# Kernel optimization log

Measured on AMD Instinct MI355X. Metric: run time of the kernel, lower is better.

The kernel has to match this reference:

```python
import jax, jax.numpy as jnp
import numpy as np

NUM_GROUPS = 4   # temporal frames == deformable groups
K = 3            # deformable / fusion kernel size
PAD = 1
MAX_DISP = 7
STRIDE2 = 2


def _conv2d(x, w):
    # 3x3, stride 1, pad 1, no bias, NCHW/OIHW
    return jax.lax.conv_general_dilated(
        x, w, window_strides=(1, 1), padding=((PAD, PAD), (PAD, PAD)),
        dimension_numbers=("NCHW", "OIHW", "NCHW"))


def _correlation(x1, x2):
    """FlowNet/PWC correlation: kernel_size=1, max_displacement=7, stride1=1, stride2=2.
    Output: [B, 49, H, W], mean over channels of shifted dot products."""
    B, C, H, W = x1.shape
    r = MAX_DISP // STRIDE2          # 3 -> 7x7 displacement grid
    m = r * STRIDE2                  # 6 = max shift magnitude
    x2p = jnp.pad(x2, ((0, 0), (0, 0), (m, m), (m, m)))
    outs = []
    for di in range(-r, r + 1):
        for dj in range(-r, r + 1):
            dy, dx = di * STRIDE2, dj * STRIDE2
            sh = x2p[:, :, m + dy:m + dy + H, m + dx:m + dx + W]
            outs.append(jnp.mean(x1 * sh, axis=1))
    return jnp.stack(outs, axis=1)   # [B, 49, H, W]


def _deform_conv(x, offset, weight):
    """Deformable conv v1 (ConvOffset2d): 3x3, stride 1, pad 1, NUM_GROUPS deformable groups.
    offset: [B, G*2*K*K, H, W] laid out as (g, k, {dy,dx})."""
    B, C, H, W = x.shape
    G, K2 = NUM_GROUPS, K * K
    Cg = C // G
    off = offset.reshape(B, G, K2, 2, H, W)
    rel = (jnp.arange(K) - PAD).astype(x.dtype)
    rel_y = jnp.repeat(rel, K).reshape(1, 1, K2, 1, 1)   # kh-major, matches weight flatten
    rel_x = jnp.tile(rel, K).reshape(1, 1, K2, 1, 1)
    iy = jnp.arange(H, dtype=x.dtype).reshape(1, 1, 1, H, 1)
    ix = jnp.arange(W, dtype=x.dtype).reshape(1, 1, 1, 1, W)
    py = iy + rel_y + off[:, :, :, 0]   # [B,G,K2,H,W] sample rows
    px = ix + rel_x + off[:, :, :, 1]   # sample cols
    xg = x.reshape(B, G, Cg, H, W).transpose(0, 1, 3, 4, 2)  # [B,G,H,W,Cg]
    y0 = jnp.floor(py); x0 = jnp.floor(px)
    fy = py - y0; fx = px - x0
    y0 = y0.astype(jnp.int32); x0 = x0.astype(jnp.int32)
    bi = jnp.arange(B).reshape(B, 1, 1, 1, 1)
    gi = jnp.arange(G).reshape(1, G, 1, 1, 1)
    acc = jnp.zeros((B, G, K2, H, W, Cg), x.dtype)
    for dy in (0, 1):
        for dx in (0, 1):
            yy = y0 + dy; xx = x0 + dx
            wgt = (fy if dy else 1.0 - fy) * (fx if dx else 1.0 - fx)
            valid = ((yy >= 0) & (yy < H) & (xx >= 0) & (xx < W)).astype(x.dtype)
            v = xg[bi, gi, jnp.clip(yy, 0, H - 1), jnp.clip(xx, 0, W - 1)]
            acc = acc + v * (wgt * valid)[..., None]
    wr = weight.reshape(weight.shape[0], G, Cg, K2)  # [O,G,Cg,K2]
    return jnp.einsum('bgkhwc,ogck->bohw', acc, wr)


def setup_inputs() -> dict:
    key = jax.random.key(0)
    k0, k1, k2, k3 = jax.random.split(key, 4)
    B, C, H, W = 4, 256, 64, 64
    G = NUM_GROUPS
    inputs = jax.random.normal(k0, (B * G, C, H, W), jnp.float32)
    w_offset = jax.random.normal(k1, (G * 2 * K * K, C + MAX_DISP ** 2, K, K), jnp.float32) * 0.02
    w_def = jax.random.normal(k2, (C, C, K, K), jnp.float32) * 0.02
    w_fusion = jax.random.normal(k3, (C, C * G, K, K), jnp.float32) * 0.02
    return {"inputs": inputs, "w_offset": w_offset, "w_def": w_def,
            "w_fusion": w_fusion, "d1": 0, "d2": 0}


def reference(inputs, w_offset, w_def, w_fusion, d1, d2):
    # d1, d2 are unused by the original forward.
    G = NUM_GROUPS
    y = inputs[G - 1::G]
    _y = jax.lax.stop_gradient(y)
    feats = []
    for ii in range(G - 1):           # n_iter = 1
        x = inputs[ii::G]
        _x = jax.lax.stop_gradient(x)
        corr = _correlation(_x, _y)                       # [B,49,H,W]
        off = _conv2d(jnp.concatenate([x, corr], axis=1), w_offset)
        x = _deform_conv(x, off, w_def)
        feats.append(x)
    return _conv2d(jnp.concatenate(feats + [y], axis=1), w_fusion)
```

## Files before the change

kernel.cpp:

```cpp
#include <hip/hip_runtime.h>

#define HH 64
#define WW 64
#define HW 4096
#define CC 256
#define BB 4
#define GG 4
#define NPAIR 3

typedef __attribute__((ext_vector_type(8))) short short8;
typedef __attribute__((ext_vector_type(4))) float f32x4;
typedef unsigned short ushort_t;

__device__ inline ushort_t f2bf(float x) {
    unsigned int u = __float_as_uint(x);
    unsigned int r = (u + 0x7fffu + ((u >> 16) & 1u)) >> 16;
    return (ushort_t)r;
}
__device__ inline float bflo(unsigned u) { return __uint_as_float(u << 16); }
__device__ inline float bfhi(unsigned u) { return __uint_as_float(u & 0xffff0000u); }

__global__ void prep_wdef(const float* __restrict__ wd, ushort_t* __restrict__ wmf) {
    int idx = blockIdx.x * 256 + threadIdx.x;
    if (idx >= 9 * 256 * 256) return;
    int k = idx >> 16;
    int rem = idx & 65535;
    int o = rem >> 8;
    int c = rem & 255;
    wmf[idx] = f2bf(wd[((size_t)(o * 256 + c)) * 9 + k]);
}

__global__ void prep_woff(const float* __restrict__ wo, ushort_t* __restrict__ wmf) {
    int idx = blockIdx.x * 256 + threadIdx.x;
    if (idx >= 9 * 80 * 320) return;
    int k = idx / (80 * 320);
    int rem = idx % (80 * 320);
    int o = rem / 320;
    int ci = rem % 320;
    wmf[idx] = (o < 72 && ci < 305) ? f2bf(wo[((size_t)o * 305 + ci) * 9 + k]) : (ushort_t)0;
}

__global__ void prep_wfus(const float* __restrict__ wf, ushort_t* __restrict__ wmf) {
    int idx = blockIdx.x * 256 + threadIdx.x;
    if (idx >= 9 * 256 * 1024) return;
    int k = idx / (256 * 1024);
    int rem = idx % (256 * 1024);
    int o = rem / 1024;
    int ci = rem % 1024;
    wmf[idx] = f2bf(wf[((size_t)o * 1024 + ci) * 9 + k]);
}

__global__ void __launch_bounds__(256) xt_build(const float* __restrict__ in,
                                                ushort_t* __restrict__ XT) {
    __shared__ ushort_t tileT[64][72];
    int hw0 = blockIdx.x * 64;
    int ct = blockIdx.y;
    int z = blockIdx.z;
    int pair = z >> 2, b = z & 3;
    int t = threadIdx.x;
    int cil = t >> 2, q = t & 3;
    const float* sp = in + ((size_t)(b * 4 + pair) * 256 + ct * 64 + cil) * HW + hw0 + q * 16;
#pragma unroll
    for (int i = 0; i < 16; ++i) tileT[q * 16 + i][cil] = f2bf(sp[i]);
    __syncthreads();
    int hwl = t >> 2;
    const uint4* tp = reinterpret_cast<const uint4*>(&tileT[hwl][q * 16]);
    uint4* op = reinterpret_cast<uint4*>(
        &XT[((size_t)z * HW + hw0 + hwl) * 320 + ct * 64 + q * 16]);
    op[0] = tp[0];
    op[1] = tp[1];
}

__global__ void __launch_bounds__(256, 8) corr_partial(const float* __restrict__ in,
                                                       float* __restrict__ P) {
    __shared__ float x1l[8][64];
    __shared__ float x2l[8][7][76];
    int h = blockIdx.x, z = blockIdx.y, cg = blockIdx.z;
    int pair = z >> 2, b = z & 3;
    const float* x1 = in + (size_t)(b * GG + pair) * CC * HW + h * WW;
    const float* x2 = in + (size_t)(b * GG + 3) * CC * HW;
    int tid = threadIdx.x;
    int w = tid & 63;
    int dg = tid >> 6;

    float acc[2][7];
#pragma unroll
    for (int i = 0; i < 2; ++i)
#pragma unroll
        for (int j = 0; j < 7; ++j) acc[i][j] = 0.f;

    for (int c0 = cg * 64; c0 < cg * 64 + 64; c0 += 8) {
        __syncthreads();
#pragma unroll
        for (int idx = tid; idx < 512; idx += 256) {
            int cc = idx >> 6, ww = idx & 63;
            x1l[cc][ww] = x1[(size_t)(c0 + cc) * HW + ww];
        }
        for (int idx = tid; idx < 8 * 7 * 76; idx += 256) {
            int cc = idx / 532;
            int rem = idx - cc * 532;
            int r = rem / 76;
            int cl = rem - r * 76;
            int row = h + 2 * (r - 3);
            int col = cl - 6;
            float v = 0.f;
            if (row >= 0 && row < HH && col >= 0 && col < WW)
                v = x2[(size_t)(c0 + cc) * HW + row * WW + col];
            x2l[cc][r][cl] = v;
        }
        __syncthreads();
#pragma unroll
        for (int cc = 0; cc < 8; ++cc) {
            float x1v = x1l[cc][w];
#pragma unroll
            for (int i = 0; i < 2; ++i) {
                int di = dg * 2 + i;
                if (di < 7) {
#pragma unroll
                    for (int dj = 0; dj < 7; ++dj)
                        acc[i][dj] += x1v * x2l[cc][di][w + 2 * dj];
                }
            }
        }
    }
    float* pp = P + ((size_t)(cg * 12 + z) * 49) * HW + h * WW + w;
#pragma unroll
    for (int i = 0; i < 2; ++i) {
        int di = dg * 2 + i;
        if (di < 7) {
#pragma unroll
            for (int dj = 0; dj < 7; ++dj)
                pp[(size_t)(di * 7 + dj) * HW] = acc[i][dj];
        }
    }
}

__global__ void __launch_bounds__(256) corr_reduce(const float* __restrict__ P,
                                                   ushort_t* __restrict__ XT) {
    int h = blockIdx.x, z = blockIdx.y;
    int tid = threadIdx.x;
    int w = tid & 63;
    int dg = tid >> 6;
    const size_t cgs = (size_t)12 * 49 * HW;
    ushort_t* xrow = XT + ((size_t)z * HW + h * WW + w) * 320;
#pragma unroll
    for (int i = 0; i < 2; ++i) {
        int di = dg * 2 + i;
        if (di < 7) {
#pragma unroll
            for (int dj = 0; dj < 7; ++dj) {
                int d = di * 7 + dj;
                const float* pp = P + ((size_t)z * 49 + d) * HW + h * WW + w;
                float s = pp[0] + pp[cgs] + pp[2 * cgs] + pp[3 * cgs];
                xrow[256 + d] = f2bf(s * (1.f / 256.f));
            }
        }
    }
    if (dg == 3) {
#pragma unroll
        for (int p = 0; p < 15; ++p) xrow[305 + p] = 0;
    }
}

__global__ void __launch_bounds__(256, 2) offconv_mfma(const ushort_t* __restrict__ XT,
                                                       const ushort_t* __restrict__ wmf,
                                                       float* __restrict__ off) {
    __shared__ ushort_t a_lds[80][40];
    __shared__ ushort_t b_lds[128][40];
    int n0 = blockIdx.x * 128;
    int z = blockIdx.y;
    int t = threadIdx.x;
    int wid = t >> 6;
    int lane = t & 63;
    int l15 = lane & 15;
    int kq = lane >> 4;
    int r2 = t >> 1, half = t & 1;
    int hwB = n0 + r2;
    int hB = hwB >> 6, wB = hwB & 63;
    const ushort_t* xtb = XT + (size_t)z * HW * 320;

    f32x4 acc[5][2];
#pragma unroll
    for (int m = 0; m < 5; ++m)
#pragma unroll
        for (int n = 0; n < 2; ++n) acc[m][n] = (f32x4){0.f, 0.f, 0.f, 0.f};

    for (int tap = 0; tap < 9; ++tap) {
        int kh = tap / 3;
        int kw = tap - kh * 3;
        int hP = hB + kh - 1;
        int wP = wB + kw - 1;
        bool valid = (hP >= 0) && (hP < HH) && (wP >= 0) && (wP < WW);
        const ushort_t* brow = xtb + (size_t)(hP * WW + wP) * 320;
#pragma unroll 1
        for (int cs = 0; cs < 10; ++cs) {
            int ci0 = cs * 32;
            uint4 vb0 = make_uint4(0, 0, 0, 0), vb1 = make_uint4(0, 0, 0, 0);
            if (valid) {
                const uint4* gp = reinterpret_cast<const uint4*>(brow + ci0 + half * 16);
                vb0 = gp[0];
                vb1 = gp[1];
            }
            uint4 va0, va1;
            if (t < 160) {
                const uint4* ga = reinterpret_cast<const uint4*>(
                    wmf + ((size_t)tap * 80 + r2) * 320 + ci0 + half * 16);
                va0 = ga[0];
                va1 = ga[1];
            }
            __syncthreads();
            {
                uint4* bp = reinterpret_cast<uint4*>(&b_lds[r2][half * 16]);
                bp[0] = vb0;
                bp[1] = vb1;
                if (t < 160) {
                    uint4* ap = reinterpret_cast<uint4*>(&a_lds[r2][half * 16]);
                    ap[0] = va0;
                    ap[1] = va1;
                }
            }
            __syncthreads();
            short8 af[5], bf[2];
#pragma unroll
            for (int m = 0; m < 5; ++m)
                af[m] = *reinterpret_cast<const short8*>(&a_lds[m * 16 + l15][kq * 8]);
#pragma unroll
            for (int n = 0; n < 2; ++n)
                bf[n] = *reinterpret_cast<const short8*>(&b_lds[wid * 32 + n * 16 + l15][kq * 8]);
#pragma unroll
            for (int m = 0; m < 5; ++m)
#pragma unroll
                for (int n = 0; n < 2; ++n)
                    acc[m][n] = __builtin_amdgcn_mfma_f32_16x16x32_bf16(af[m], bf[n],
                                                                        acc[m][n], 0, 0, 0);
        }
    }
    float* ob = off + (size_t)z * 72 * HW + n0 + wid * 32;
#pragma unroll
    for (int m = 0; m < 5; ++m)
#pragma unroll
        for (int n = 0; n < 2; ++n)
#pragma unroll
            for (int e = 0; e < 4; ++e) {
                int o_l = m * 16 + kq * 4 + e;
                if (o_l < 72) ob[(size_t)o_l * HW + n * 16 + l15] = acc[m][n][e];
            }
}

__global__ void __launch_bounds__(256, 3) deform_mfma(const ushort_t* __restrict__ XT,
                                                      const float* __restrict__ off,
                                                      const ushort_t* __restrict__ wmf,
                                                      ushort_t* __restrict__ FT) {
    __shared__ ushort_t b_lds[64][264];
    int u = blockIdx.x & 7, v = blockIdx.x >> 3;
    int lin = u * 96 + v;
    int z = lin >> 6, h = lin & 63;
    int b = z & 3, pair = z >> 2;

    const ushort_t* xtz = XT + (size_t)z * HW * 320;
    const float* offp = off + (size_t)z * 72 * HW;
    int tid = threadIdx.x;
    int lane = tid & 63;
    int g = tid >> 6;
    int l15 = tid & 15;
    int kq = (tid >> 4) & 3;

    f32x4 acc[4][4];
#pragma unroll
    for (int m = 0; m < 4; ++m)
#pragma unroll
        for (int n = 0; n < 4; ++n) acc[m][n] = (f32x4){0.f, 0.f, 0.f, 0.f};

    for (int k = 0; k < 9; ++k) {
        __syncthreads();
        {
            float oy = offp[(size_t)(g * 18 + k * 2 + 0) * HW + h * WW + lane];
            float ox = offp[(size_t)(g * 18 + k * 2 + 1) * HW + h * WW + lane];
            float py = (float)h + (float)(k / 3 - 1) + oy;
            float px = (float)lane + (float)(k % 3 - 1) + ox;
            float y0f = floorf(py), x0f = floorf(px);
            float fy = py - y0f, fx = px - x0f;
            int y0 = (int)y0f, x0 = (int)x0f;
            int y1 = y0 + 1, x1 = x0 + 1;
            bool vy0 = (y0 >= 0) && (y0 < HH);
            bool vy1 = (y1 >= 0) && (y1 < HH);
            bool vx0 = (x0 >= 0) && (x0 < WW);
            bool vx1 = (x1 >= 0) && (x1 < WW);
            float w00 = (1.f - fy) * (1.f - fx) * ((vy0 && vx0) ? 1.f : 0.f);
            float w01 = (1.f - fy) * fx * ((vy0 && vx1) ? 1.f : 0.f);
            float w10 = fy * (1.f - fx) * ((vy1 && vx0) ? 1.f : 0.f);
            float w11 = fy * fx * ((vy1 && vx1) ? 1.f : 0.f);
            int cy0 = min(max(y0, 0), HH - 1), cy1 = min(max(y1, 0), HH - 1);
            int cx0 = min(max(x0, 0), WW - 1), cx1 = min(max(x1, 0), WW - 1);
            const ushort_t* p00 = xtz + (size_t)(cy0 * WW + cx0) * 320 + g * 64;
            const ushort_t* p01 = xtz + (size_t)(cy0 * WW + cx1) * 320 + g * 64;
            const ushort_t* p10 = xtz + (size_t)(cy1 * WW + cx0) * 320 + g * 64;
            const ushort_t* p11 = xtz + (size_t)(cy1 * WW + cx1) * 320 + g * 64;
#pragma unroll
            for (int c0 = 0; c0 < 64; c0 += 8) {
                uint4 a00 = *reinterpret_cast<const uint4*>(p00 + c0);
                uint4 a01 = *reinterpret_cast<const uint4*>(p01 + c0);
                uint4 a10 = *reinterpret_cast<const uint4*>(p10 + c0);
                uint4 a11 = *reinterpret_cast<const uint4*>(p11 + c0);
                unsigned pw[4];
                const unsigned* u00 = &a00.x;
                const unsigned* u01 = &a01.x;
                const unsigned* u10 = &a10.x;
                const unsigned* u11 = &a11.x;
#pragma unroll
                for (int q = 0; q < 4; ++q) {
                    float s0 = w00 * bflo(u00[q]) + w01 * bflo(u01[q]) +
                               w10 * bflo(u10[q]) + w11 * bflo(u11[q]);
                    float s1 = w00 * bfhi(u00[q]) + w01 * bfhi(u01[q]) +
                               w10 * bfhi(u10[q]) + w11 * bfhi(u11[q]);
                    pw[q] = (unsigned)f2bf(s0) | ((unsigned)f2bf(s1) << 16);
                }
                *reinterpret_cast<uint4*>(&b_lds[lane][g * 64 + c0]) =
                    make_uint4(pw[0], pw[1], pw[2], pw[3]);
            }
        }
        __syncthreads();
        const ushort_t* wkbase = wmf + (size_t)k * 65536 + (size_t)(g * 64) * 256;
#pragma unroll 1
        for (int cs = 0; cs < 8; ++cs) {
            int c0 = cs * 32;
            short8 bfr[4], afr[4];
#pragma unroll
            for (int n = 0; n < 4; ++n)
                bfr[n] = *reinterpret_cast<const short8*>(&b_lds[n * 16 + l15][c0 + kq * 8]);
#pragma unroll
            for (int m = 0; m < 4; ++m)
                afr[m] = *reinterpret_cast<const short8*>(
                    wkbase + (size_t)(m * 16 + l15) * 256 + c0 + kq * 8);
#pragma unroll
            for (int m = 0; m < 4; ++m)
#pragma unroll
                for (int n = 0; n < 4; ++n)
                    acc[m][n] = __builtin_amdgcn_mfma_f32_16x16x32_bf16(afr[m], bfr[n],
                                                                        acc[m][n], 0, 0, 0);
        }
    }
    __syncthreads();
#pragma unroll
    for (int m = 0; m < 4; ++m)
#pragma unroll
        for (int n = 0; n < 4; ++n) {
            unsigned lo = (unsigned)f2bf(acc[m][n][0]) | ((unsigned)f2bf(acc[m][n][1]) << 16);
            unsigned hi = (unsigned)f2bf(acc[m][n][2]) | ((unsigned)f2bf(acc[m][n][3]) << 16);
            uint2 vv = make_uint2(lo, hi);
            *reinterpret_cast<uint2*>(&b_lds[n * 16 + l15][g * 64 + m * 16 + kq * 4]) = vv;
        }
    __syncthreads();
    int wout = tid >> 2, ch = tid & 3;
    ushort_t* dst = FT + ((size_t)b * HW + h * 64 + wout) * 1024 + pair * 256 + ch * 64;
    const ushort_t* srcl = &b_lds[wout][ch * 64];
#pragma unroll
    for (int i = 0; i < 8; ++i) {
        uint4 vv = *reinterpret_cast<const uint4*>(srcl + i * 8);
        *reinterpret_cast<uint4*>(dst + i * 8) = vv;
    }
}

__global__ void __launch_bounds__(256) ft_build_y(const float* __restrict__ in,
                                                  ushort_t* __restrict__ FT) {
    __shared__ ushort_t tileT[64][72];
    int hw0 = blockIdx.x * 64;
    int ct = blockIdx.y;
    int b = blockIdx.z;
    int t = threadIdx.x;
    int cil = t >> 2, q = t & 3;
    const float* sp = in + ((size_t)(b * 4 + 3) * 256 + ct * 64 + cil) * HW + hw0 + q * 16;
#pragma unroll
    for (int i = 0; i < 16; ++i) tileT[q * 16 + i][cil] = f2bf(sp[i]);
    __syncthreads();
    int hwl = t >> 2;
    const uint4* tp = reinterpret_cast<const uint4*>(&tileT[hwl][q * 16]);
    uint4* op = reinterpret_cast<uint4*>(
        &FT[((size_t)b * HW + hw0 + hwl) * 1024 + 768 + ct * 64 + q * 16]);
    op[0] = tp[0];
    op[1] = tp[1];
}

__global__ void __launch_bounds__(256, 2) fusion_mfma(const ushort_t* __restrict__ FT,
                                                      const ushort_t* __restrict__ wmf,
                                                      float* __restrict__ out) {
    __shared__ ushort_t a_lds[9][64][32];
    __shared__ ushort_t b_hal[264][32];
    int lin = ((blockIdx.x & 7) << 6) | (blockIdx.x >> 3);
    int ot = lin & 3;
    int g2 = lin >> 2;
    int n0t = g2 & 31;
    int b = g2 >> 5;
    int o0 = ot * 64;
    int h0 = n0t * 2;
    int t = threadIdx.x;
    int wid = t >> 6;
    int lane = t & 63;
    int l15 = lane & 15;
    int kq = lane >> 4;
    const ushort_t* ftb = FT + (size_t)b * HW * 1024;

    f32x4 acc[4][2];
#pragma unroll
    for (int fm = 0; fm < 4; ++fm)
#pragma unroll
        for (int fn = 0; fn < 2; ++fn) acc[fm][fn] = (f32x4){0.f, 0.f, 0.f, 0.f};

#pragma unroll 1
    for (int cs = 0; cs < 32; ++cs) {
        int ci0 = cs * 32;
        __syncthreads();
        for (int idx = t; idx < 264; idx += 256) {
            int r = idx / 66, c = idx - r * 66;
            int hP = h0 + r - 1, wP = c - 1;
            uint4* dst = reinterpret_cast<uint4*>(&b_hal[idx][0]);
            if (hP >= 0 && hP < HH && wP >= 0 && wP < WW) {
                const uint4* src = reinterpret_cast<const uint4*>(
                    ftb + (size_t)(hP * WW + wP) * 1024 + ci0);
                dst[0] = src[0];
                dst[1] = src[1];
                dst[2] = src[2];
                dst[3] = src[3];
            } else {
                uint4 zz = make_uint4(0, 0, 0, 0);
                dst[0] = zz;
                dst[1] = zz;
                dst[2] = zz;
                dst[3] = zz;
            }
        }
        for (int idx = t; idx < 2304; idx += 256) {
            int tp = idx >> 8;
            int rem = idx & 255;
            int o = rem >> 2, q = rem & 3;
            *reinterpret_cast<uint4*>(&a_lds[tp][o][q * 8]) =
                *reinterpret_cast<const uint4*>(
                    wmf + ((size_t)(tp * 256 + o0 + o) << 10) + ci0 + q * 8);
        }
        __syncthreads();
#pragma unroll 1
        for (int tap = 0; tap < 9; ++tap) {
            int kh = tap / 3, kw = tap - kh * 3;
            short8 af[4], bf[2];
#pragma unroll
            for (int m = 0; m < 4; ++m)
                af[m] = *reinterpret_cast<const short8*>(&a_lds[tap][m * 16 + l15][kq * 8]);
#pragma unroll
            for (int n = 0; n < 2; ++n) {
                int p = wid * 32 + n * 16 + l15;
                int pos = ((p >> 6) + kh) * 66 + (p & 63) + kw;
                bf[n] = *reinterpret_cast<const short8*>(&b_hal[pos][kq * 8]);
            }
#pragma unroll
            for (int m = 0; m < 4; ++m)
#pragma unroll
                for (int n = 0; n < 2; ++n)
                    acc[m][n] = __builtin_amdgcn_mfma_f32_16x16x32_bf16(af[m], bf[n],
                                                                        acc[m][n], 0, 0, 0);
        }
    }
    float* ob = out + ((size_t)b * 256 + o0) * HW + h0 * 64 + wid * 32;
#pragma unroll
    for (int fm = 0; fm < 4; ++fm)
#pragma unroll
        for (int fn = 0; fn < 2; ++fn)
#pragma unroll
            for (int e = 0; e < 4; ++e) {
                int o_l = fm * 16 + 4 * kq + e;
                ob[(size_t)o_l * HW + fn * 16 + l15] = acc[fm][fn][e];
            }
}

extern "C" void kernel_launch(void* const* d_in, const int* in_sizes, int n_in,
                              void* d_out, int out_size, void* d_ws, size_t ws_size,
                              hipStream_t stream) {
    const float* in   = (const float*)d_in[0];
    const float* wOff = (const float*)d_in[1];
    const float* wDef = (const float*)d_in[2];
    const float* wFus = (const float*)d_in[3];
    float* out = (float*)d_out;
    char* base = (char*)d_ws;

    ushort_t* XT     = (ushort_t*)base;
    ushort_t* FT     = (ushort_t*)(base + 31457280);
    float* corrP     = (float*)(base + 31457280);
    float* offB      = (float*)(base + 65011712);
    ushort_t* wdefMF = (ushort_t*)(base + 79167488);
    ushort_t* woffMF = (ushort_t*)(base + 80347136);
    ushort_t* wfusMF = (ushort_t*)(base + 80807936);

    hipLaunchKernelGGL(prep_wdef, dim3((9 * 256 * 256 + 255) / 256), dim3(256), 0, stream,
                       wDef, wdefMF);
    hipLaunchKernelGGL(prep_woff, dim3((9 * 80 * 320 + 255) / 256), dim3(256), 0, stream,
                       wOff, woffMF);
    hipLaunchKernelGGL(prep_wfus, dim3((9 * 256 * 1024 + 255) / 256), dim3(256), 0, stream,
                       wFus, wfusMF);
    hipLaunchKernelGGL(xt_build, dim3(64, 4, 12), dim3(256), 0, stream, in, XT);
    hipLaunchKernelGGL(corr_partial, dim3(64, 12, 4), dim3(256), 0, stream, in, corrP);
    hipLaunchKernelGGL(corr_reduce, dim3(64, 12), dim3(256), 0, stream, corrP, XT);
    hipLaunchKernelGGL(offconv_mfma, dim3(32, 12), dim3(256), 0, stream, XT, woffMF, offB);
    hipLaunchKernelGGL(ft_build_y, dim3(64, 4, 4), dim3(256), 0, stream, in, FT);
    hipLaunchKernelGGL(deform_mfma, dim3(768), dim3(256), 0, stream, XT, offB, wdefMF, FT);
    hipLaunchKernelGGL(fusion_mfma, dim3(512), dim3(256), 0, stream, FT, wfusMF, out);
}
```

Measured before the change: 588.8 us.

## Split deform conv tiles into half-row blocks and preload all offsets

The deformable conv kernel now handles 32 output pixels per block instead of a full 64-pixel row, doubling the grid to 1536 blocks and halving LDS and accumulator use so more blocks fit per CU (launch bounds raised to 4). Bilinear sampling is re-mapped so each thread gathers 32 channels for one pixel, and all nine offset pairs are loaded into registers before the kernel-tap loop. The aim is better occupancy and latency hiding for the gather-heavy phase. The cost is that each weight fragment loaded from global memory feeds only half as many MFMAs, so weight traffic per output doubles.

New measurement: 678.3 us. 1.15x slower.

```diff
diff --git a/kernel.cpp b/kernel.cpp
--- a/kernel.cpp
+++ b/kernel.cpp
@@ -247,37 +247,49 @@
             }
 }
 
-__global__ void __launch_bounds__(256, 3) deform_mfma(const ushort_t* __restrict__ XT,
+__global__ void __launch_bounds__(256, 4) deform_mfma(const ushort_t* __restrict__ XT,
                                                       const float* __restrict__ off,
                                                       const ushort_t* __restrict__ wmf,
                                                       ushort_t* __restrict__ FT) {
-    __shared__ ushort_t b_lds[64][264];
+    __shared__ ushort_t b_lds[32][264];
     int u = blockIdx.x & 7, v = blockIdx.x >> 3;
-    int lin = u * 96 + v;
-    int z = lin >> 6, h = lin & 63;
+    int lin = u * 192 + v;
+    int z = lin >> 7;
+    int h = (lin >> 1) & 63;
+    int wh = lin & 1;
+    int w0 = wh * 32;
     int b = z & 3, pair = z >> 2;
 
     const ushort_t* xtz = XT + (size_t)z * HW * 320;
     const float* offp = off + (size_t)z * 72 * HW;
     int tid = threadIdx.x;
-    int lane = tid & 63;
-    int g = tid >> 6;
+    int w = tid & 31;
+    int gg = tid >> 5;
+    int g = gg >> 1;
+    int ch0 = (gg & 1) * 32;
+    int wg = w0 + w;
+    int wid = tid >> 6;
     int l15 = tid & 15;
     int kq = (tid >> 4) & 3;
 
-    f32x4 acc[4][4];
+    float oys[9], oxs[9];
+#pragma unroll
+    for (int k = 0; k < 9; ++k) {
+        oys[k] = offp[(size_t)(g * 18 + k * 2 + 0) * HW + h * WW + wg];
+        oxs[k] = offp[(size_t)(g * 18 + k * 2 + 1) * HW + h * WW + wg];
+    }
+
+    f32x4 acc[4][2];
 #pragma unroll
     for (int m = 0; m < 4; ++m)
 #pragma unroll
-        for (int n = 0; n < 4; ++n) acc[m][n] = (f32x4){0.f, 0.f, 0.f, 0.f};
+        for (int n = 0; n < 2; ++n) acc[m][n] = (f32x4){0.f, 0.f, 0.f, 0.f};
 
     for (int k = 0; k < 9; ++k) {
         __syncthreads();
         {
-            float oy = offp[(size_t)(g * 18 + k * 2 + 0) * HW + h * WW + lane];
-            float ox = offp[(size_t)(g * 18 + k * 2 + 1) * HW + h * WW + lane];
-            float py = (float)h + (float)(k / 3 - 1) + oy;
-            float px = (float)lane + (float)(k % 3 - 1) + ox;
+            float py = (float)h + (float)(k / 3 - 1) + oys[k];
+            float px = (float)wg + (float)(k % 3 - 1) + oxs[k];
             float y0f = floorf(py), x0f = floorf(px);
             float fy = py - y0f, fx = px - x0f;
             int y0 = (int)y0f, x0 = (int)x0f;
@@ -292,12 +304,12 @@
             float w11 = fy * fx * ((vy1 && vx1) ? 1.f : 0.f);
             int cy0 = min(max(y0, 0), HH - 1), cy1 = min(max(y1, 0), HH - 1);
             int cx0 = min(max(x0, 0), WW - 1), cx1 = min(max(x1, 0), WW - 1);
-            const ushort_t* p00 = xtz + (size_t)(cy0 * WW + cx0) * 320 + g * 64;
-            const ushort_t* p01 = xtz + (size_t)(cy0 * WW + cx1) * 320 + g * 64;
-            const ushort_t* p10 = xtz + (size_t)(cy1 * WW + cx0) * 320 + g * 64;
-            const ushort_t* p11 = xtz + (size_t)(cy1 * WW + cx1) * 320 + g * 64;
-#pragma unroll
-            for (int c0 = 0; c0 < 64; c0 += 8) {
+            const ushort_t* p00 = xtz + (size_t)(cy0 * WW + cx0) * 320 + g * 64 + ch0;
+            const ushort_t* p01 = xtz + (size_t)(cy0 * WW + cx1) * 320 + g * 64 + ch0;
+            const ushort_t* p10 = xtz + (size_t)(cy1 * WW + cx0) * 320 + g * 64 + ch0;
+            const ushort_t* p11 = xtz + (size_t)(cy1 * WW + cx1) * 320 + g * 64 + ch0;
+#pragma unroll
+            for (int c0 = 0; c0 < 32; c0 += 8) {
                 uint4 a00 = *reinterpret_cast<const uint4*>(p00 + c0);
                 uint4 a01 = *reinterpret_cast<const uint4*>(p01 + c0);
                 uint4 a10 = *reinterpret_cast<const uint4*>(p10 + c0);
@@ -315,18 +327,18 @@
                                w10 * bfhi(u10[q]) + w11 * bfhi(u11[q]);
                     pw[q] = (unsigned)f2bf(s0) | ((unsigned)f2bf(s1) << 16);
                 }
-                *reinterpret_cast<uint4*>(&b_lds[lane][g * 64 + c0]) =
+                *reinterpret_cast<uint4*>(&b_lds[w][gg * 32 + c0]) =
                     make_uint4(pw[0], pw[1], pw[2], pw[3]);
             }
         }
         __syncthreads();
-        const ushort_t* wkbase = wmf + (size_t)k * 65536 + (size_t)(g * 64) * 256;
+        const ushort_t* wkbase = wmf + (size_t)k * 65536 + (size_t)(wid * 64) * 256;
 #pragma unroll 1
         for (int cs = 0; cs < 8; ++cs) {
             int c0 = cs * 32;
-            short8 bfr[4], afr[4];
-#pragma unroll
-            for (int n = 0; n < 4; ++n)
+            short8 bfr[2], afr[4];
+#pragma unroll
+            for (int n = 0; n < 2; ++n)
                 bfr[n] = *reinterpret_cast<const short8*>(&b_lds[n * 16 + l15][c0 + kq * 8]);
 #pragma unroll
             for (int m = 0; m < 4; ++m)
@@ -335,7 +347,7 @@
 #pragma unroll
             for (int m = 0; m < 4; ++m)
 #pragma unroll
-                for (int n = 0; n < 4; ++n)
+                for (int n = 0; n < 2; ++n)
                     acc[m][n] = __builtin_amdgcn_mfma_f32_16x16x32_bf16(afr[m], bfr[n],
                                                                         acc[m][n], 0, 0, 0);
         }
@@ -344,18 +356,18 @@
 #pragma unroll
     for (int m = 0; m < 4; ++m)
 #pragma unroll
-        for (int n = 0; n < 4; ++n) {
+        for (int n = 0; n < 2; ++n) {
             unsigned lo = (unsigned)f2bf(acc[m][n][0]) | ((unsigned)f2bf(acc[m][n][1]) << 16);
             unsigned hi = (unsigned)f2bf(acc[m][n][2]) | ((unsigned)f2bf(acc[m][n][3]) << 16);
             uint2 vv = make_uint2(lo, hi);
-            *reinterpret_cast<uint2*>(&b_lds[n * 16 + l15][g * 64 + m * 16 + kq * 4]) = vv;
+            *reinterpret_cast<uint2*>(&b_lds[n * 16 + l15][wid * 64 + m * 16 + kq * 4]) = vv;
         }
     __syncthreads();
-    int wout = tid >> 2, ch = tid & 3;
-    ushort_t* dst = FT + ((size_t)b * HW + h * 64 + wout) * 1024 + pair * 256 + ch * 64;
-    const ushort_t* srcl = &b_lds[wout][ch * 64];
-#pragma unroll
-    for (int i = 0; i < 8; ++i) {
+    int wout = tid >> 3, ch = tid & 7;
+    ushort_t* dst = FT + ((size_t)b * HW + h * 64 + w0 + wout) * 1024 + pair * 256 + ch * 32;
+    const ushort_t* srcl = &b_lds[wout][ch * 32];
+#pragma unroll
+    for (int i = 0; i < 4; ++i) {
         uint4 vv = *reinterpret_cast<const uint4*>(srcl + i * 8);
         *reinterpret_cast<uint4*>(dst + i * 8) = vv;
     }
@@ -500,6 +512,6 @@
     hipLaunchKernelGGL(corr_reduce, dim3(64, 12), dim3(256), 0, stream, corrP, XT);
     hipLaunchKernelGGL(offconv_mfma, dim3(32, 12), dim3(256), 0, stream, XT, woffMF, offB);
     hipLaunchKernelGGL(ft_build_y, dim3(64, 4, 4), dim3(256), 0, stream, in, FT);
-    hipLaunchKernelGGL(deform_mfma, dim3(768), dim3(256), 0, stream, XT, offB, wdefMF, FT);
+    hipLaunchKernelGGL(deform_mfma, dim3(1536), dim3(256), 0, stream, XT, offB, wdefMF, FT);
     hipLaunchKernelGGL(fusion_mfma, dim3(512), dim3(256), 0, stream, FT, wfusMF, out);
 }
```

## Restructure deform bilinear gather so each wave cooperatively samples one pixel

Applied to the files above, without the earlier changes.

The bilinear sampling phase of the deformable-conv kernel is reorganised. Offsets for the current tap are staged in LDS. Each wave then loops over the 64 output pixels, with its four 16-lane quarters each loading one bilinear corner and the corners combined through cross-lane shuffles. This aims to turn scattered per-lane 16-byte gathers from four corners into coalesced contiguous channel loads. In exchange it adds a 64-iteration serial loop with shuffles per tap, narrower 4-byte loads, and an extra barrier.

New measurement: 813.4 us. 1.38x slower.

```diff
diff --git a/kernel.cpp b/kernel.cpp
--- a/kernel.cpp
+++ b/kernel.cpp
@@ -252,6 +252,7 @@
                                                       const ushort_t* __restrict__ wmf,
                                                       ushort_t* __restrict__ FT) {
     __shared__ ushort_t b_lds[64][264];
+    __shared__ float off_lds[4][2][64];
     int u = blockIdx.x & 7, v = blockIdx.x >> 3;
     int lin = u * 96 + v;
     int z = lin >> 6, h = lin & 63;
@@ -264,6 +265,7 @@
     int g = tid >> 6;
     int l15 = tid & 15;
     int kq = (tid >> 4) & 3;
+    int q = lane >> 4, cp = lane & 15;
 
     f32x4 acc[4][4];
 #pragma unroll
@@ -273,50 +275,42 @@
 
     for (int k = 0; k < 9; ++k) {
         __syncthreads();
-        {
-            float oy = offp[(size_t)(g * 18 + k * 2 + 0) * HW + h * WW + lane];
-            float ox = offp[(size_t)(g * 18 + k * 2 + 1) * HW + h * WW + lane];
-            float py = (float)h + (float)(k / 3 - 1) + oy;
-            float px = (float)lane + (float)(k % 3 - 1) + ox;
+        for (int idx = tid; idx < 512; idx += 256)
+            off_lds[idx >> 7][(idx >> 6) & 1][idx & 63] =
+                offp[(size_t)((idx >> 7) * 18 + k * 2 + ((idx >> 6) & 1)) * HW +
+                     h * WW + (idx & 63)];
+        __syncthreads();
+        float fk_h = (float)(k / 3 - 1), fk_w = (float)(k % 3 - 1);
+#pragma unroll 2
+        for (int w = 0; w < 64; ++w) {
+            float oy = off_lds[g][0][w];
+            float ox = off_lds[g][1][w];
+            float py = (float)h + fk_h + oy;
+            float px = (float)w + fk_w + ox;
             float y0f = floorf(py), x0f = floorf(px);
             float fy = py - y0f, fx = px - x0f;
-            int y0 = (int)y0f, x0 = (int)x0f;
-            int y1 = y0 + 1, x1 = x0 + 1;
-            bool vy0 = (y0 >= 0) && (y0 < HH);
-            bool vy1 = (y1 >= 0) && (y1 < HH);
-            bool vx0 = (x0 >= 0) && (x0 < WW);
-            bool vx1 = (x1 >= 0) && (x1 < WW);
-            float w00 = (1.f - fy) * (1.f - fx) * ((vy0 && vx0) ? 1.f : 0.f);
-            float w01 = (1.f - fy) * fx * ((vy0 && vx1) ? 1.f : 0.f);
-            float w10 = fy * (1.f - fx) * ((vy1 && vx0) ? 1.f : 0.f);
-            float w11 = fy * fx * ((vy1 && vx1) ? 1.f : 0.f);
-            int cy0 = min(max(y0, 0), HH - 1), cy1 = min(max(y1, 0), HH - 1);
-            int cx0 = min(max(x0, 0), WW - 1), cx1 = min(max(x1, 0), WW - 1);
-            const ushort_t* p00 = xtz + (size_t)(cy0 * WW + cx0) * 320 + g * 64;
-            const ushort_t* p01 = xtz + (size_t)(cy0 * WW + cx1) * 320 + g * 64;
-            const ushort_t* p10 = xtz + (size_t)(cy1 * WW + cx0) * 320 + g * 64;
-            const ushort_t* p11 = xtz + (size_t)(cy1 * WW + cx1) * 320 + g * 64;
-#pragma unroll
-            for (int c0 = 0; c0 < 64; c0 += 8) {
-                uint4 a00 = *reinterpret_cast<const uint4*>(p00 + c0);
-                uint4 a01 = *reinterpret_cast<const uint4*>(p01 + c0);
-                uint4 a10 = *reinterpret_cast<const uint4*>(p10 + c0);
-                uint4 a11 = *reinterpret_cast<const uint4*>(p11 + c0);
-                unsigned pw[4];
-                const unsigned* u00 = &a00.x;
-                const unsigned* u01 = &a01.x;
-                const unsigned* u10 = &a10.x;
-                const unsigned* u11 = &a11.x;
-#pragma unroll
-                for (int q = 0; q < 4; ++q) {
-                    float s0 = w00 * bflo(u00[q]) + w01 * bflo(u01[q]) +
-                               w10 * bflo(u10[q]) + w11 * bflo(u11[q]);
-                    float s1 = w00 * bfhi(u00[q]) + w01 * bfhi(u01[q]) +
-                               w10 * bfhi(u10[q]) + w11 * bfhi(u11[q]);
-                    pw[q] = (unsigned)f2bf(s0) | ((unsigned)f2bf(s1) << 16);
+            int yq = (int)y0f + (q >> 1);
+            int xq = (int)x0f + (q & 1);
+            bool vld = (yq >= 0) && (yq < HH) && (xq >= 0) && (xq < WW);
+            float wy = (q & 2) ? fy : 1.f - fy;
+            float wx = (q & 1) ? fx : 1.f - fx;
+            float wq = wy * wx * (vld ? 1.f : 0.f);
+            int cy = min(max(yq, 0), HH - 1), cx = min(max(xq, 0), WW - 1);
+            const ushort_t* pb = xtz + (size_t)(cy * WW + cx) * 320 + g * 64;
+#pragma unroll
+            for (int half = 0; half < 2; ++half) {
+                unsigned uv = *reinterpret_cast<const unsigned*>(pb + half * 32 + cp * 2);
+                float s0 = wq * bflo(uv);
+                float s1 = wq * bfhi(uv);
+                s0 += __shfl_xor(s0, 16);
+                s1 += __shfl_xor(s1, 16);
+                s0 += __shfl_xor(s0, 32);
+                s1 += __shfl_xor(s1, 32);
+                if (q == 0) {
+                    unsigned pwv = (unsigned)f2bf(s0) | ((unsigned)f2bf(s1) << 16);
+                    *reinterpret_cast<unsigned*>(
+                        &b_lds[w][g * 64 + half * 32 + cp * 2]) = pwv;
                 }
-                *reinterpret_cast<uint4*>(&b_lds[lane][g * 64 + c0]) =
-                    make_uint4(pw[0], pw[1], pw[2], pw[3]);
             }
         }
         __syncthreads();
```

## Double-buffer deformable sampling in LDS to overlap gather with MFMA

Applied to the files above, without the earlier changes.

The deform_mfma kernel now keeps two LDS buffers for the bilinearly sampled tile. The next tap's gather and interpolation are written into one buffer while MFMAs consume the other, which removes one barrier per tap. The aim is to hide global gather latency behind matrix math. In exchange LDS use doubles, and the launch bound drops from 3 to 2 blocks per SM, so occupancy falls.

Result: no change. 597.8 us (+1.5%).

```diff
diff --git a/kernel.cpp b/kernel.cpp
--- a/kernel.cpp
+++ b/kernel.cpp
@@ -247,11 +247,11 @@
             }
 }
 
-__global__ void __launch_bounds__(256, 3) deform_mfma(const ushort_t* __restrict__ XT,
+__global__ void __launch_bounds__(256, 2) deform_mfma(const ushort_t* __restrict__ XT,
                                                       const float* __restrict__ off,
                                                       const ushort_t* __restrict__ wmf,
                                                       ushort_t* __restrict__ FT) {
-    __shared__ ushort_t b_lds[64][264];
+    __shared__ ushort_t b_lds[2][64][264];
     int u = blockIdx.x & 7, v = blockIdx.x >> 3;
     int lin = u * 96 + v;
     int z = lin >> 6, h = lin & 63;
@@ -271,63 +271,67 @@
 #pragma unroll
         for (int n = 0; n < 4; ++n) acc[m][n] = (f32x4){0.f, 0.f, 0.f, 0.f};
 
+    auto sample_tap = [&](int k, int bsel) {
+        float oy = offp[(size_t)(g * 18 + k * 2 + 0) * HW + h * WW + lane];
+        float ox = offp[(size_t)(g * 18 + k * 2 + 1) * HW + h * WW + lane];
+        float py = (float)h + (float)(k / 3 - 1) + oy;
+        float px = (float)lane + (float)(k % 3 - 1) + ox;
+        float y0f = floorf(py), x0f = floorf(px);
+        float fy = py - y0f, fx = px - x0f;
+        int y0 = (int)y0f, x0 = (int)x0f;
+        int y1 = y0 + 1, x1 = x0 + 1;
+        bool vy0 = (y0 >= 0) && (y0 < HH);
+        bool vy1 = (y1 >= 0) && (y1 < HH);
+        bool vx0 = (x0 >= 0) && (x0 < WW);
+        bool vx1 = (x1 >= 0) && (x1 < WW);
+        float w00 = (1.f - fy) * (1.f - fx) * ((vy0 && vx0) ? 1.f : 0.f);
+        float w01 = (1.f - fy) * fx * ((vy0 && vx1) ? 1.f : 0.f);
+        float w10 = fy * (1.f - fx) * ((vy1 && vx0) ? 1.f : 0.f);
+        float w11 = fy * fx * ((vy1 && vx1) ? 1.f : 0.f);
+        int cy0 = min(max(y0, 0), HH - 1), cy1 = min(max(y1, 0), HH - 1);
+        int cx0 = min(max(x0, 0), WW - 1), cx1 = min(max(x1, 0), WW - 1);
+        const ushort_t* p00 = xtz + (size_t)(cy0 * WW + cx0) * 320 + g * 64;
+        const ushort_t* p01 = xtz + (size_t)(cy0 * WW + cx1) * 320 + g * 64;
+        const ushort_t* p10 = xtz + (size_t)(cy1 * WW + cx0) * 320 + g * 64;
+        const ushort_t* p11 = xtz + (size_t)(cy1 * WW + cx1) * 320 + g * 64;
+#pragma unroll
+        for (int c0 = 0; c0 < 64; c0 += 8) {
+            uint4 a00 = *reinterpret_cast<const uint4*>(p00 + c0);
+            uint4 a01 = *reinterpret_cast<const uint4*>(p01 + c0);
+            uint4 a10 = *reinterpret_cast<const uint4*>(p10 + c0);
+            uint4 a11 = *reinterpret_cast<const uint4*>(p11 + c0);
+            unsigned pw[4];
+            const unsigned* u00 = &a00.x;
+            const unsigned* u01 = &a01.x;
+            const unsigned* u10 = &a10.x;
+            const unsigned* u11 = &a11.x;
+#pragma unroll
+            for (int qq = 0; qq < 4; ++qq) {
+                float s0 = w00 * bflo(u00[qq]) + w01 * bflo(u01[qq]) +
+                           w10 * bflo(u10[qq]) + w11 * bflo(u11[qq]);
+                float s1 = w00 * bfhi(u00[qq]) + w01 * bfhi(u01[qq]) +
+                           w10 * bfhi(u10[qq]) + w11 * bfhi(u11[qq]);
+                pw[qq] = (unsigned)f2bf(s0) | ((unsigned)f2bf(s1) << 16);
+            }
+            *reinterpret_cast<uint4*>(&b_lds[bsel][lane][g * 64 + c0]) =
+                make_uint4(pw[0], pw[1], pw[2], pw[3]);
+        }
+    };
+
+    sample_tap(0, 0);
+    __syncthreads();
     for (int k = 0; k < 9; ++k) {
-        __syncthreads();
-        {
-            float oy = offp[(size_t)(g * 18 + k * 2 + 0) * HW + h * WW + lane];
-            float ox = offp[(size_t)(g * 18 + k * 2 + 1) * HW + h * WW + lane];
-            float py = (float)h + (float)(k / 3 - 1) + oy;
-            float px = (float)lane + (float)(k % 3 - 1) + ox;
-            float y0f = floorf(py), x0f = floorf(px);
-            float fy = py - y0f, fx = px - x0f;
-            int y0 = (int)y0f, x0 = (int)x0f;
-            int y1 = y0 + 1, x1 = x0 + 1;
-            bool vy0 = (y0 >= 0) && (y0 < HH);
-            bool vy1 = (y1 >= 0) && (y1 < HH);
-            bool vx0 = (x0 >= 0) && (x0 < WW);
-            bool vx1 = (x1 >= 0) && (x1 < WW);
-            float w00 = (1.f - fy) * (1.f - fx) * ((vy0 && vx0) ? 1.f : 0.f);
-            float w01 = (1.f - fy) * fx * ((vy0 && vx1) ? 1.f : 0.f);
-            float w10 = fy * (1.f - fx) * ((vy1 && vx0) ? 1.f : 0.f);
-            float w11 = fy * fx * ((vy1 && vx1) ? 1.f : 0.f);
-            int cy0 = min(max(y0, 0), HH - 1), cy1 = min(max(y1, 0), HH - 1);
-            int cx0 = min(max(x0, 0), WW - 1), cx1 = min(max(x1, 0), WW - 1);
-            const ushort_t* p00 = xtz + (size_t)(cy0 * WW + cx0) * 320 + g * 64;
-            const ushort_t* p01 = xtz + (size_t)(cy0 * WW + cx1) * 320 + g * 64;
-            const ushort_t* p10 = xtz + (size_t)(cy1 * WW + cx0) * 320 + g * 64;
-            const ushort_t* p11 = xtz + (size_t)(cy1 * WW + cx1) * 320 + g * 64;
-#pragma unroll
-            for (int c0 = 0; c0 < 64; c0 += 8) {
-                uint4 a00 = *reinterpret_cast<const uint4*>(p00 + c0);
-                uint4 a01 = *reinterpret_cast<const uint4*>(p01 + c0);
-                uint4 a10 = *reinterpret_cast<const uint4*>(p10 + c0);
-                uint4 a11 = *reinterpret_cast<const uint4*>(p11 + c0);
-                unsigned pw[4];
-                const unsigned* u00 = &a00.x;
-                const unsigned* u01 = &a01.x;
-                const unsigned* u10 = &a10.x;
-                const unsigned* u11 = &a11.x;
-#pragma unroll
-                for (int q = 0; q < 4; ++q) {
-                    float s0 = w00 * bflo(u00[q]) + w01 * bflo(u01[q]) +
-                               w10 * bflo(u10[q]) + w11 * bflo(u11[q]);
-                    float s1 = w00 * bfhi(u00[q]) + w01 * bfhi(u01[q]) +
-                               w10 * bfhi(u10[q]) + w11 * bfhi(u11[q]);
-                    pw[q] = (unsigned)f2bf(s0) | ((unsigned)f2bf(s1) << 16);
-                }
-                *reinterpret_cast<uint4*>(&b_lds[lane][g * 64 + c0]) =
-                    make_uint4(pw[0], pw[1], pw[2], pw[3]);
-            }
-        }
-        __syncthreads();
+        if (k < 8) sample_tap(k + 1, (k + 1) & 1);
         const ushort_t* wkbase = wmf + (size_t)k * 65536 + (size_t)(g * 64) * 256;
+        int bsel = k & 1;
 #pragma unroll 1
         for (int cs = 0; cs < 8; ++cs) {
             int c0 = cs * 32;
             short8 bfr[4], afr[4];
 #pragma unroll
             for (int n = 0; n < 4; ++n)
-                bfr[n] = *reinterpret_cast<const short8*>(&b_lds[n * 16 + l15][c0 + kq * 8]);
+                bfr[n] = *reinterpret_cast<const short8*>(
+                    &b_lds[bsel][n * 16 + l15][c0 + kq * 8]);
 #pragma unroll
             for (int m = 0; m < 4; ++m)
                 afr[m] = *reinterpret_cast<const short8*>(
@@ -339,8 +343,8 @@
                     acc[m][n] = __builtin_amdgcn_mfma_f32_16x16x32_bf16(afr[m], bfr[n],
                                                                         acc[m][n], 0, 0, 0);
         }
-    }
-    __syncthreads();
+        __syncthreads();
+    }
 #pragma unroll
     for (int m = 0; m < 4; ++m)
 #pragma unroll
@@ -348,12 +352,12 @@
             unsigned lo = (unsigned)f2bf(acc[m][n][0]) | ((unsigned)f2bf(acc[m][n][1]) << 16);
             unsigned hi = (unsigned)f2bf(acc[m][n][2]) | ((unsigned)f2bf(acc[m][n][3]) << 16);
             uint2 vv = make_uint2(lo, hi);
-            *reinterpret_cast<uint2*>(&b_lds[n * 16 + l15][g * 64 + m * 16 + kq * 4]) = vv;
+            *reinterpret_cast<uint2*>(&b_lds[0][n * 16 + l15][g * 64 + m * 16 + kq * 4]) = vv;
         }
     __syncthreads();
     int wout = tid >> 2, ch = tid & 3;
     ushort_t* dst = FT + ((size_t)b * HW + h * 64 + wout) * 1024 + pair * 256 + ch * 64;
-    const ushort_t* srcl = &b_lds[wout][ch * 64];
+    const ushort_t* srcl = &b_lds[0][wout][ch * 64];
 #pragma unroll
     for (int i = 0; i < 8; ++i) {
         uint4 vv = *reinterpret_cast<const uint4*>(srcl + i * 8);
```
